# Kernel tuning notes

Hardware: AMD Instinct MI355X
Metric: run time of the kernel (lower is better)

The kernel has to match this reference:

```python
import jax, jax.numpy as jnp
import numpy as np

N_NODES = 50000
N_EDGES = 800000
ATOM_DIM = 128
BOND_DIM = 16
HID = 128
STEPS = 4


def setup_inputs() -> dict:
    key = jax.random.key(0)
    k1, k2, k3, k4, k5, k6 = jax.random.split(key, 6)
    atoms = jax.random.normal(k1, (N_NODES, ATOM_DIM), dtype=jnp.float32)
    bonds = jax.random.normal(k2, (N_NODES, BOND_DIM), dtype=jnp.float32)
    pairs = jax.random.randint(k3, (N_EDGES, 2), 0, N_NODES)
    # sort rows by target id (tf.math.segment_sum expects sorted segment ids)
    order = jnp.argsort(pairs[:, 0])
    pairs = pairs[order].astype(jnp.int64)
    # learned parameters (glorot-ish scaling)
    kernel = jax.random.normal(k4, (ATOM_DIM, BOND_DIM * BOND_DIM), dtype=jnp.float32) * (2.0 / (ATOM_DIM + BOND_DIM * BOND_DIM)) ** 0.5
    bias = jnp.zeros((BOND_DIM * BOND_DIM,), dtype=jnp.float32)
    weight_node = jax.random.normal(k5, (BOND_DIM, HID), dtype=jnp.float32) * (2.0 / (BOND_DIM + HID)) ** 0.5
    weight_node_inp = jax.random.normal(k6, (BOND_DIM, HID), dtype=jnp.float32) * (2.0 / (BOND_DIM + HID)) ** 0.5
    return {"atoms": atoms, "bonds": bonds, "pairs": pairs,
            "kernel": kernel, "bias": bias,
            "weight_node": weight_node, "weight_node_inp": weight_node_inp}


def reference(atoms, bonds, pairs, kernel, bias, weight_node, weight_node_inp):
    n, bd = bonds.shape
    # per-node transform -> [N, bd, bd] message matrices
    A = (atoms @ kernel + bias).reshape(n, bd, bd)
    src = pairs[:, 0]
    nbr = pairs[:, 1]
    # gather bonds of neighbors, apply source-node matrix per edge: [E, bd]
    trans = jnp.einsum('eij,ej->ei', A[src], bonds[nbr])
    # scatter-add back to nodes keyed on pairs[:,0]
    aggregate = jax.ops.segment_sum(trans, src, num_segments=n)  # [N, bd]
    # step loop: aggregate is never updated in the original, so each step
    # computes the identical result; compute once and replicate.
    nodes = aggregate @ weight_node            # [N, hid]
    edges = jax.nn.relu(bonds @ weight_node_inp)  # [N, hid]
    result = jax.nn.relu(nodes + edges)
    return jnp.stack([result] * STEPS)  # [steps, N, hid]
```

## Files before the change

kernel.cpp:

```cpp
#include <hip/hip_runtime.h>

typedef __attribute__((ext_vector_type(8))) short bf16x8;
typedef __attribute__((ext_vector_type(4))) float f32x4;

constexpr int N       = 50000;
constexpr int NE      = 800000;
constexpr int AD      = 128;
constexpr int BD      = 16;
constexpr int BD2     = 256;
constexpr int HIDDEN  = 128;
constexpr int NBS     = 32;
constexpr int NBE     = 64;
constexpr int SSTR    = 20;
constexpr int OSTR    = 132;

__device__ inline short f2bf(float f) {
    union U { float f; unsigned u; } v; v.f = f;
    unsigned r = v.u + 0x7fffu + ((v.u >> 16) & 1u);
    return (short)(r >> 16);
}

__global__ __launch_bounds__(256) void prep_frags(
    const float* __restrict__ kmat,
    const float* __restrict__ Wn,
    const float* __restrict__ Wi,
    short* __restrict__ kbf,
    short* __restrict__ wbf)
{
    int t = blockIdx.x * 256 + threadIdx.x;
    if (t < 4096) {
        int u = t >> 6, l = t & 63;
        int nf = u >> 2, kk = u & 3;
        int col = nf * 16 + (l & 15);
        int k0  = kk * 32 + (l >> 4) * 8;
        bf16x8 o;
#pragma unroll
        for (int j = 0; j < 8; ++j) o[j] = f2bf(kmat[(size_t)(k0 + j) * BD2 + col]);
        *(bf16x8*)(kbf + (size_t)t * 8) = o;
    } else if (t < 4096 + 1024) {
        int t2 = t - 4096;
        int u = t2 >> 6, l = t2 & 63;
        int m = u >> 3, nf2 = u & 7;
        const float* W = m ? Wi : Wn;
        int col = nf2 * 16 + (l & 15);
        int k0  = (l >> 4) * 8;
        bf16x8 o;
#pragma unroll
        for (int j = 0; j < 8; ++j) {
            int k = k0 + j;
            o[j] = (k < 16) ? f2bf(W[(size_t)k * HIDDEN + col]) : (short)0;
        }
        *(bf16x8*)(wbf + (size_t)t2 * 8) = o;
    }
}

__global__ __launch_bounds__(256) void scatter_tile(
    const int*  __restrict__ pairs,
    const float* __restrict__ bonds,
    float* __restrict__ S)
{
    __shared__ float st[NBS * SSTR];

    const int tid = threadIdx.x;
    const int nb  = blockIdx.x * NBS;

    for (int i = tid; i < NBS * SSTR; i += 256) st[i] = 0.f;

    int wlo = nb * 16 - 4096; if (wlo < 0) wlo = 0;
    int whi = (nb + NBS) * 16 + 4096; if (whi > NE) whi = NE;
    if (wlo > 0  && pairs[2 * wlo] >= nb)       wlo = 0;
    if (whi < NE && pairs[2 * whi] <  nb + NBS) whi = NE;
    int eLo, eHi;
    {
        int s = wlo, e = whi;
        while (s < e) { int m = (s + e) >> 1; if (pairs[2 * m] < nb) s = m + 1; else e = m; }
        eLo = s;
    }
    {
        int s = eLo, e = whi;
        while (s < e) { int m = (s + e) >> 1; if (pairs[2 * m] < nb + NBS) s = m + 1; else e = m; }
        eHi = s;
    }
    __syncthreads();

    {
        const int g = tid >> 4;
        const int c = tid & 15;
        const int nE = eHi - eLo;
        const int cg = (nE + 15) >> 4;
        int gs = eLo + g * cg;
        int ge = gs + cg; if (ge > eHi) ge = eHi;
        int cur = -1; float acc = 0.f;
        int e = gs;
        for (; e + 4 <= ge; e += 4) {
            int2 pb[4]; float vb[4];
#pragma unroll
            for (int i = 0; i < 4; ++i) pb[i] = *(const int2*)(pairs + 2 * (e + i));
#pragma unroll
            for (int i = 0; i < 4; ++i) vb[i] = bonds[(size_t)pb[i].y * BD + c];
#pragma unroll
            for (int i = 0; i < 4; ++i) {
                if (pb[i].x != cur) {
                    if (cur >= 0) atomicAdd(&st[(cur - nb) * SSTR + c], acc);
                    acc = 0.f; cur = pb[i].x;
                }
                acc += vb[i];
            }
        }
        for (; e < ge; ++e) {
            int2 p = *(const int2*)(pairs + 2 * e);
            float v = bonds[(size_t)p.y * BD + c];
            if (p.x != cur) {
                if (cur >= 0) atomicAdd(&st[(cur - nb) * SSTR + c], acc);
                acc = 0.f; cur = p.x;
            }
            acc += v;
        }
        if (cur >= 0) atomicAdd(&st[(cur - nb) * SSTR + c], acc);
    }
    __syncthreads();

    if (tid < NBS * 4) {
        int node = tid >> 2;
        int c4   = (tid & 3) * 4;
        if (nb + node < N) {
            f32x4 v = *(const f32x4*)(&st[node * SSTR + c4]);
            *(f32x4*)(S + (size_t)(nb + node) * BD + c4) = v;
        }
    }
}

__global__ __launch_bounds__(256, 4) void gemm_contract(
    const float* __restrict__ atoms,
    const short* __restrict__ kbf,
    const float* __restrict__ bias,
    const float* __restrict__ S,
    float* __restrict__ agg)
{
    __shared__ float ag[NBS * SSTR];

    const int tid = threadIdx.x;
    const int w   = tid >> 6;
    const int l   = tid & 63;
    const int lq  = l >> 4;
    const int lj  = l & 15;
    const int nb  = blockIdx.x * NBS;

    bf16x8 afrag[2][4];
    float4 sval[2];
#pragma unroll
    for (int ng = 0; ng < 2; ++ng) {
        int arow = nb + ng * 16 + lj; if (arow >= N) arow = N - 1;
        const float* ap = atoms + (size_t)arow * AD + lq * 8;
        sval[ng] = *(const float4*)(S + (size_t)arow * BD + lq * 4);
#pragma unroll
        for (int kk = 0; kk < 4; ++kk) {
            float4 a0 = *(const float4*)(ap + kk * 32);
            float4 a1 = *(const float4*)(ap + kk * 32 + 4);
            bf16x8 t;
            t[0] = f2bf(a0.x); t[1] = f2bf(a0.y); t[2] = f2bf(a0.z); t[3] = f2bf(a0.w);
            t[4] = f2bf(a1.x); t[5] = f2bf(a1.y); t[6] = f2bf(a1.z); t[7] = f2bf(a1.w);
            afrag[ng][kk] = t;
        }
    }

    const bf16x8* kb = (const bf16x8*)kbf;
    float aggf[2][4];
#pragma unroll
    for (int nfl = 0; nfl < 4; ++nfl) {
        const int nf = w * 4 + nfl;
        bf16x8 b[4];
#pragma unroll
        for (int kk = 0; kk < 4; ++kk)
            b[kk] = kb[(size_t)(nf * 4 + kk) * 64 + l];
        f32x4 acc[2];
#pragma unroll
        for (int ng = 0; ng < 2; ++ng) acc[ng] = (f32x4){0.f, 0.f, 0.f, 0.f};
#pragma unroll
        for (int kk = 0; kk < 4; ++kk) {
#pragma unroll
            for (int ng = 0; ng < 2; ++ng)
                acc[ng] = __builtin_amdgcn_mfma_f32_16x16x32_bf16(
                    b[kk], afrag[ng][kk], acc[ng], 0, 0, 0);
        }
        float4 bv = *(const float4*)(bias + nf * 16 + lq * 4);
#pragma unroll
        for (int ng = 0; ng < 2; ++ng) {
            float q = (acc[ng][0] + bv.x) * sval[ng].x
                    + (acc[ng][1] + bv.y) * sval[ng].y
                    + (acc[ng][2] + bv.z) * sval[ng].z
                    + (acc[ng][3] + bv.w) * sval[ng].w;
            q += __shfl_xor(q, 16);
            q += __shfl_xor(q, 32);
            aggf[ng][nfl] = q;
        }
    }

#pragma unroll
    for (int ng = 0; ng < 2; ++ng) {
        float v = aggf[ng][0];
        v = (lq == 1) ? aggf[ng][1] : v;
        v = (lq == 2) ? aggf[ng][2] : v;
        v = (lq == 3) ? aggf[ng][3] : v;
        ag[(ng * 16 + lj) * SSTR + w * 4 + lq] = v;
    }
    __syncthreads();

    if (tid < NBS * 4) {
        int node = tid >> 2;
        int c4   = (tid & 3) * 4;
        if (nb + node < N) {
            f32x4 v = *(const f32x4*)(&ag[node * SSTR + c4]);
            *(f32x4*)(agg + (size_t)(nb + node) * BD + c4) = v;
        }
    }
}

__global__ __launch_bounds__(256) void epilogue_store(
    const float* __restrict__ agg,
    const float* __restrict__ bonds,
    const short* __restrict__ wbf,
    float* __restrict__ out)
{
    __shared__ float lds[NBE * OSTR];

    const int tid = threadIdx.x;
    const int w   = tid >> 6;
    const int l   = tid & 63;
    const int lq  = l >> 4;
    const int lj  = l & 15;
    const int nb  = blockIdx.x * NBE;
    const int cp  = blockIdx.y;
    const int wrow = nb + w * 16;

    int arow = wrow + lj; if (arow >= N) arow = N - 1;

    bf16x8 agg_a  = (bf16x8){0,0,0,0,0,0,0,0};
    bf16x8 bond_a = (bf16x8){0,0,0,0,0,0,0,0};
    {
        int half = lq & 1;
        float4 g0 = *(const float4*)(agg   + (size_t)arow * BD + half * 8);
        float4 g1 = *(const float4*)(agg   + (size_t)arow * BD + half * 8 + 4);
        float4 b0 = *(const float4*)(bonds + (size_t)arow * BD + half * 8);
        float4 b1 = *(const float4*)(bonds + (size_t)arow * BD + half * 8 + 4);
        if (lq < 2) {
            agg_a[0] = f2bf(g0.x); agg_a[1] = f2bf(g0.y); agg_a[2] = f2bf(g0.z); agg_a[3] = f2bf(g0.w);
            agg_a[4] = f2bf(g1.x); agg_a[5] = f2bf(g1.y); agg_a[6] = f2bf(g1.z); agg_a[7] = f2bf(g1.w);
            bond_a[0] = f2bf(b0.x); bond_a[1] = f2bf(b0.y); bond_a[2] = f2bf(b0.z); bond_a[3] = f2bf(b0.w);
            bond_a[4] = f2bf(b1.x); bond_a[5] = f2bf(b1.y); bond_a[6] = f2bf(b1.z); bond_a[7] = f2bf(b1.w);
        }
    }

    const bf16x8* wb = (const bf16x8*)wbf;
#pragma unroll
    for (int nf2 = 0; nf2 < 8; ++nf2) {
        bf16x8 wn_f = wb[(size_t)nf2 * 64 + l];
        bf16x8 wi_f = wb[(size_t)(8 + nf2) * 64 + l];
        f32x4 e = __builtin_amdgcn_mfma_f32_16x16x32_bf16(
            bond_a, wi_f, (f32x4){0.f, 0.f, 0.f, 0.f}, 0, 0, 0);
        e[0] = fmaxf(e[0], 0.f); e[1] = fmaxf(e[1], 0.f);
        e[2] = fmaxf(e[2], 0.f); e[3] = fmaxf(e[3], 0.f);
        f32x4 o = __builtin_amdgcn_mfma_f32_16x16x32_bf16(agg_a, wn_f, e, 0, 0, 0);
#pragma unroll
        for (int r = 0; r < 4; ++r) {
            int nl = w * 16 + 4 * lq + r;
            lds[nl * OSTR + nf2 * 16 + lj] = fmaxf(o[r], 0.f);
        }
    }
    __syncthreads();

#pragma unroll
    for (int p = 0; p < 8; ++p) {
        int idx  = tid + 256 * p;
        int nl   = idx >> 5;
        int h4   = (idx & 31) * 4;
        int node = nb + nl;
        if (node < N) {
            f32x4 v = *(const f32x4*)(&lds[nl * OSTR + h4]);
            *(f32x4*)(out + ((size_t)cp * N + node) * HIDDEN + h4) = v;
        }
    }
}

extern "C" void kernel_launch(void* const* d_in, const int* in_sizes, int n_in,
                              void* d_out, int out_size, void* d_ws, size_t ws_size,
                              hipStream_t stream)
{
    const float* atoms = (const float*)d_in[0];
    const float* bonds = (const float*)d_in[1];
    const int*   pairs = (const int*)d_in[2];
    const float* kmat  = (const float*)d_in[3];
    const float* bias  = (const float*)d_in[4];
    const float* Wn    = (const float*)d_in[5];
    const float* Wi    = (const float*)d_in[6];
    float* out = (float*)d_out;

    short* kbf  = (short*)d_ws;
    short* wbf  = kbf + 4096 * 8;
    float* Sagg = (float*)(wbf + 1024 * 8);

    const int nblk32 = (N + NBS - 1) / NBS;
    const int nblk64 = (N + NBE - 1) / NBE;

    prep_frags<<<20, 256, 0, stream>>>(kmat, Wn, Wi, kbf, wbf);
    scatter_tile<<<nblk32, 256, 0, stream>>>(pairs, bonds, Sagg);
    gemm_contract<<<nblk32, 256, 0, stream>>>(atoms, kbf, bias, Sagg, Sagg);
    epilogue_store<<<dim3(nblk64, 4), 256, 0, stream>>>(Sagg, bonds, wbf, out);
}
```

Measured before the change: 85.06 us.

## Replace node-tiled binary-search scatter with edge-parallel global atomic segment sum

Replaces the per-node-tile scatter kernel, which binary-searched edge ranges and reduced into shared memory, with an edge-parallel kernel. In the new kernel each 16-lane group handles a fixed chunk of 32 sorted edges, run-length accumulates per target, and flushes with global atomicAdd into a buffer zeroed by a memset. This removes the search overhead and the load imbalance between tiles, but adds global atomics, one memset, and nondeterministic float summation order. Pairs are read as int2, which treats the int64 input as int32 pairs, the same reinterpretation the old kernel already made.

```diff
diff --git a/kernel.cpp b/kernel.cpp
--- a/kernel.cpp
+++ b/kernel.cpp
@@ -9,6 +9,7 @@
 constexpr int BD      = 16;
 constexpr int BD2     = 256;
 constexpr int HIDDEN  = 128;
+constexpr int EPG     = 32;
 constexpr int NBS     = 32;
 constexpr int NBE     = 64;
 constexpr int SSTR    = 20;
@@ -54,88 +55,42 @@
     }
 }
 
-__global__ __launch_bounds__(256) void scatter_tile(
-    const int*  __restrict__ pairs,
+__global__ __launch_bounds__(256) void edge_scatter_sorted(
+    const int2* __restrict__ pairs,
     const float* __restrict__ bonds,
     float* __restrict__ S)
 {
-    __shared__ float st[NBS * SSTR];
-
-    const int tid = threadIdx.x;
-    const int nb  = blockIdx.x * NBS;
-
-    for (int i = tid; i < NBS * SSTR; i += 256) st[i] = 0.f;
-
-    int wlo = nb * 16 - 4096; if (wlo < 0) wlo = 0;
-    int whi = (nb + NBS) * 16 + 4096; if (whi > NE) whi = NE;
-    if (wlo > 0  && pairs[2 * wlo] >= nb)       wlo = 0;
-    if (whi < NE && pairs[2 * whi] <  nb + NBS) whi = NE;
-    int eLo, eHi;
-    {
-        int s = wlo, e = whi;
-        while (s < e) { int m = (s + e) >> 1; if (pairs[2 * m] < nb) s = m + 1; else e = m; }
-        eLo = s;
-    }
-    {
-        int s = eLo, e = whi;
-        while (s < e) { int m = (s + e) >> 1; if (pairs[2 * m] < nb + NBS) s = m + 1; else e = m; }
-        eHi = s;
-    }
-    __syncthreads();
-
-    {
-        const int g = tid >> 4;
-        const int c = tid & 15;
-        const int nE = eHi - eLo;
-        const int cg = (nE + 15) >> 4;
-        int gs = eLo + g * cg;
-        int ge = gs + cg; if (ge > eHi) ge = eHi;
-        int cur = -1; float acc = 0.f;
-        int e = gs;
-        for (; e + 4 <= ge; e += 4) {
-            int2 pb[4]; float vb[4];
-#pragma unroll
-            for (int i = 0; i < 4; ++i) pb[i] = *(const int2*)(pairs + 2 * (e + i));
-#pragma unroll
-            for (int i = 0; i < 4; ++i) vb[i] = bonds[(size_t)pb[i].y * BD + c];
-#pragma unroll
-            for (int i = 0; i < 4; ++i) {
-                if (pb[i].x != cur) {
-                    if (cur >= 0) atomicAdd(&st[(cur - nb) * SSTR + c], acc);
-                    acc = 0.f; cur = pb[i].x;
-                }
-                acc += vb[i];
+    const int gid = (int)((blockIdx.x * (unsigned)blockDim.x + threadIdx.x) >> 4);
+    const int c   = threadIdx.x & 15;
+    long e0 = (long)gid * EPG;
+    if (e0 >= NE) return;
+
+    int   cur = -1;
+    float acc = 0.f;
+    for (long e = e0; e < e0 + EPG; e += 4) {
+        int2 pb[4]; float vb[4];
+#pragma unroll
+        for (int i = 0; i < 4; ++i) pb[i] = pairs[e + i];
+#pragma unroll
+        for (int i = 0; i < 4; ++i) vb[i] = bonds[(size_t)pb[i].y * BD + c];
+#pragma unroll
+        for (int i = 0; i < 4; ++i) {
+            if (pb[i].x != cur) {
+                if (cur >= 0) atomicAdd(&S[(size_t)cur * BD + c], acc);
+                acc = 0.f;
+                cur = pb[i].x;
             }
-        }
-        for (; e < ge; ++e) {
-            int2 p = *(const int2*)(pairs + 2 * e);
-            float v = bonds[(size_t)p.y * BD + c];
-            if (p.x != cur) {
-                if (cur >= 0) atomicAdd(&st[(cur - nb) * SSTR + c], acc);
-                acc = 0.f; cur = p.x;
-            }
-            acc += v;
-        }
-        if (cur >= 0) atomicAdd(&st[(cur - nb) * SSTR + c], acc);
-    }
-    __syncthreads();
-
-    if (tid < NBS * 4) {
-        int node = tid >> 2;
-        int c4   = (tid & 3) * 4;
-        if (nb + node < N) {
-            f32x4 v = *(const f32x4*)(&st[node * SSTR + c4]);
-            *(f32x4*)(S + (size_t)(nb + node) * BD + c4) = v;
-        }
-    }
+            acc += vb[i];
+        }
+    }
+    atomicAdd(&S[(size_t)cur * BD + c], acc);
 }
 
 __global__ __launch_bounds__(256, 4) void gemm_contract(
     const float* __restrict__ atoms,
     const short* __restrict__ kbf,
     const float* __restrict__ bias,
-    const float* __restrict__ S,
-    float* __restrict__ agg)
+    float* Sagg)
 {
     __shared__ float ag[NBS * SSTR];
 
@@ -152,7 +107,7 @@
     for (int ng = 0; ng < 2; ++ng) {
         int arow = nb + ng * 16 + lj; if (arow >= N) arow = N - 1;
         const float* ap = atoms + (size_t)arow * AD + lq * 8;
-        sval[ng] = *(const float4*)(S + (size_t)arow * BD + lq * 4);
+        sval[ng] = *(const float4*)(Sagg + (size_t)arow * BD + lq * 4);
 #pragma unroll
         for (int kk = 0; kk < 4; ++kk) {
             float4 a0 = *(const float4*)(ap + kk * 32);
@@ -211,7 +166,7 @@
         int c4   = (tid & 3) * 4;
         if (nb + node < N) {
             f32x4 v = *(const f32x4*)(&ag[node * SSTR + c4]);
-            *(f32x4*)(agg + (size_t)(nb + node) * BD + c4) = v;
+            *(f32x4*)(Sagg + (size_t)(nb + node) * BD + c4) = v;
         }
     }
 }
@@ -288,7 +243,7 @@
 {
     const float* atoms = (const float*)d_in[0];
     const float* bonds = (const float*)d_in[1];
-    const int*   pairs = (const int*)d_in[2];
+    const int2*  pairs = (const int2*)d_in[2];
     const float* kmat  = (const float*)d_in[3];
     const float* bias  = (const float*)d_in[4];
     const float* Wn    = (const float*)d_in[5];
@@ -302,8 +257,13 @@
     const int nblk32 = (N + NBS - 1) / NBS;
     const int nblk64 = (N + NBE - 1) / NBE;
 
+    hipMemsetAsync(Sagg, 0, (size_t)N * BD * sizeof(float), stream);
     prep_frags<<<20, 256, 0, stream>>>(kmat, Wn, Wi, kbf, wbf);
-    scatter_tile<<<nblk32, 256, 0, stream>>>(pairs, bonds, Sagg);
-    gemm_contract<<<nblk32, 256, 0, stream>>>(atoms, kbf, bias, Sagg, Sagg);
+
+    const int groups  = NE / EPG;
+    const int threads = groups * 16;
+    edge_scatter_sorted<<<(threads + 255) / 256, 256, 0, stream>>>(pairs, bonds, Sagg);
+
+    gemm_contract<<<nblk32, 256, 0, stream>>>(atoms, kbf, bias, Sagg);
     epilogue_store<<<dim3(nblk64, 4), 256, 0, stream>>>(Sagg, bonds, wbf, out);
 }
```

Result: slower. 96.00 us (+12.9%).
